# Performance work log

Hardware: AMD Instinct MI355X
Metric: run time of the kernel (lower is better)

## Reference

```python
import jax, jax.numpy as jnp
import numpy as np

B, N, D = 8, 1024, 768      # batch, n_patches, prototype dim
V, C, Hh = 30000, 512, 768  # vocab size, clip_text_dim, proj hidden dim
TEMPERATURE = 0.2
BN_EPS = 1e-5


def _l2norm(x, axis=-1, eps=1e-12):
    # matches torch F.normalize (clamp_min on the norm)
    n = jnp.linalg.norm(x, axis=axis, keepdims=True)
    return x / jnp.maximum(n, eps)


def setup_inputs() -> dict:
    key = jax.random.key(0)
    k = jax.random.split(key, 6)
    patch_tokens = jax.random.normal(k[0], (B, N, D), dtype=jnp.float32)
    vocab_clip_embeddings = jax.random.normal(k[1], (V, C), dtype=jnp.float32)
    # ProjectionHead params: Linear(C->Hh, no bias) + BN(Hh) + ReLU + Linear(Hh->D, bias)
    W1 = jax.random.normal(k[2], (C, Hh), dtype=jnp.float32) / np.sqrt(C)
    bn_gamma = jnp.ones((Hh,), dtype=jnp.float32)
    bn_beta = jnp.zeros((Hh,), dtype=jnp.float32)
    W2 = jax.random.normal(k[3], (Hh, D), dtype=jnp.float32) / np.sqrt(Hh)
    b2 = jnp.zeros((D,), dtype=jnp.float32)
    return {
        "patch_tokens": patch_tokens,
        "vocab_clip_embeddings": vocab_clip_embeddings,
        "W1": W1,
        "bn_gamma": bn_gamma,
        "bn_beta": bn_beta,
        "W2": W2,
        "b2": b2,
    }


def reference(patch_tokens, vocab_clip_embeddings, W1, bn_gamma, bn_beta, W2, b2):
    # vocab CLIP embeddings are L2-normalized at module init
    vocab = _l2norm(vocab_clip_embeddings)            # [V, C]
    # ProjectionHead (training-mode BatchNorm over the V "batch" dim)
    h = vocab @ W1                                    # [V, Hh]
    mean = jnp.mean(h, axis=0)
    var = jnp.var(h, axis=0)                          # biased, as torch BN uses
    h = (h - mean) * (bn_gamma / jnp.sqrt(var + BN_EPS)) + bn_beta
    h = jax.nn.relu(h)
    prototypes = _l2norm(h @ W2 + b2)                 # [V, D]
    # normalize patch tokens, compute patch-prototype logits
    pt = _l2norm(patch_tokens)                        # [B, N, D]
    patch_prototype_logits = jnp.einsum("bnd,vd->bnv", pt, prototypes)  # [B, N, V]
    vocab_logits = jnp.max(patch_prototype_logits, axis=1)              # [B, V]
    mixture_weights = jax.nn.softmax(vocab_logits / TEMPERATURE, axis=-1)
    return mixture_weights
```

## Files before the change

kernel.cpp:

```cpp
#include <hip/hip_runtime.h>
#include <hip/hip_bf16.h>
#include <cstdint>


#define CDIV(a,b) (((a)+(b)-1)/(b))

using bf16x8 = __attribute__((ext_vector_type(8))) __bf16;
using f32x4  = __attribute__((ext_vector_type(4))) float;

__device__ __forceinline__ unsigned short f2bf(float x) {
  unsigned u = __float_as_uint(x);
  u += 0x7fffu + ((u >> 16) & 1u);
  return (unsigned short)(u >> 16);
}
__device__ __forceinline__ float bf2f(unsigned short b) {
  return __uint_as_float(((unsigned)b) << 16);
}
__device__ __forceinline__ unsigned fkey(float x) {
  unsigned u = __float_as_uint(x);
  return (u & 0x80000000u) ? ~u : (u | 0x80000000u);
}
__device__ __forceinline__ float fdec(unsigned k) {
  unsigned u = (k & 0x80000000u) ? (k ^ 0x80000000u) : ~k;
  return __uint_as_float(u);
}

__global__ __launch_bounds__(512, 1)
void gemm256_max_kernel(const unsigned short* __restrict__ A,
                        const unsigned short* __restrict__ B,
                        unsigned* __restrict__ maxkey)
{
  constexpr int K = 768, NT = 12, NXT = 118;
  __shared__ __align__(16) unsigned short lds[8 * 8192];

  const int tid = threadIdx.x;
  const int w = tid >> 6, lane = tid & 63;
  const int lr = lane & 15, kg = lane >> 4;
  const int wr = w >> 2, wc = w & 3;

  const int bid = blockIdx.x;
  const int wg = (bid & 7) * 472 + (bid >> 3);
  const long m0 = (long)(wg / NXT) * 256;
  const long n0 = (long)(wg % NXT) * 256;

  auto stage = [&](int slot, int tk, int mat, int h) {
    const unsigned short* src = mat ? B : A;
    const long row0 = mat ? n0 : m0;
    unsigned short* dst = lds + (((slot * 2) + mat) * 2 + h) * 8192;
#pragma unroll
    for (int ld = 0; ld < 2; ++ld) {
      const int lc  = ld * 512 + tid;
      const int row = lc >> 2;
      const int qc  = (lc & 3) ^ ((row >> 1) & 3);
      const unsigned short* gp = src + (row0 + row) * K + tk * 64 + h * 32 + qc * 8;
      __builtin_amdgcn_global_load_lds(
          (const __attribute__((address_space(1))) void*)gp,
          (__attribute__((address_space(3))) void*)(dst + (ld * 512 + (w << 6)) * 8),
          16, 0, 0);
    }
  };
  auto rdA = [&](int s, int h, int fm) -> bf16x8 {
    const int row = wr * 128 + fm * 16 + lr;
    const int pc  = kg ^ ((row >> 1) & 3);
    return *(const bf16x8*)(lds + ((s * 2 + 0) * 2 + h) * 8192 + row * 32 + pc * 8);
  };
  auto rdB = [&](int s, int h, int fn) -> bf16x8 {
    const int row = wc * 64 + fn * 16 + lr;
    const int pc  = kg ^ ((row >> 1) & 3);
    return *(const bf16x8*)(lds + ((s * 2 + 1) * 2 + h) * 8192 + row * 32 + pc * 8);
  };

  f32x4 acc[8][4];
#pragma unroll
  for (int i = 0; i < 8; ++i)
#pragma unroll
    for (int j = 0; j < 4; ++j) acc[i][j] = f32x4{0.f, 0.f, 0.f, 0.f};

  stage(0, 0, 0, 0); stage(0, 0, 1, 0); stage(0, 0, 0, 1);
  stage(0, 0, 1, 1); stage(1, 1, 0, 0); stage(1, 1, 1, 0);
  asm volatile("s_waitcnt vmcnt(8)" ::: "memory");
  __builtin_amdgcn_s_barrier();

  bf16x8 a[4], b[4];
  auto tile_body = [&](int t, int s) {
    const int t1c = (t + 1 < NT) ? t + 1 : NT - 1;
    const int t2c = (t + 2 < NT) ? t + 2 : NT - 1;
    const int s1  = s ^ 1;

#pragma unroll
    for (int i = 0; i < 4; ++i) a[i] = rdA(s, 0, i);
#pragma unroll
    for (int i = 0; i < 4; ++i) b[i] = rdB(s, 0, i);
    stage(s1, t1c, 0, 1);
    __builtin_amdgcn_s_barrier();
    asm volatile("s_waitcnt lgkmcnt(0)" ::: "memory");
    __builtin_amdgcn_sched_barrier(0);
    __builtin_amdgcn_s_setprio(1);
#pragma unroll
    for (int fm = 0; fm < 4; ++fm)
#pragma unroll
      for (int fn = 0; fn < 4; ++fn)
        acc[fm][fn] = __builtin_amdgcn_mfma_f32_16x16x32_bf16(a[fm], b[fn], acc[fm][fn], 0, 0, 0);
    __builtin_amdgcn_s_setprio(0);
    __builtin_amdgcn_sched_barrier(0);
    __builtin_amdgcn_s_barrier();

#pragma unroll
    for (int i = 0; i < 4; ++i) a[i] = rdA(s, 0, 4 + i);
    stage(s1, t1c, 1, 1);
    __builtin_amdgcn_s_barrier();
    asm volatile("s_waitcnt lgkmcnt(0)" ::: "memory");
    __builtin_amdgcn_sched_barrier(0);
    __builtin_amdgcn_s_setprio(1);
#pragma unroll
    for (int fm = 0; fm < 4; ++fm)
#pragma unroll
      for (int fn = 0; fn < 4; ++fn)
        acc[4 + fm][fn] = __builtin_amdgcn_mfma_f32_16x16x32_bf16(a[fm], b[fn], acc[4 + fm][fn], 0, 0, 0);
    __builtin_amdgcn_s_setprio(0);
    asm volatile("s_waitcnt vmcnt(8)" ::: "memory");
    __builtin_amdgcn_sched_barrier(0);
    __builtin_amdgcn_s_barrier();

#pragma unroll
    for (int i = 0; i < 4; ++i) a[i] = rdA(s, 1, i);
#pragma unroll
    for (int i = 0; i < 4; ++i) b[i] = rdB(s, 1, i);
    stage(s, t2c, 0, 0);
    __builtin_amdgcn_s_barrier();
    asm volatile("s_waitcnt lgkmcnt(0)" ::: "memory");
    __builtin_amdgcn_sched_barrier(0);
    __builtin_amdgcn_s_setprio(1);
#pragma unroll
    for (int fm = 0; fm < 4; ++fm)
#pragma unroll
      for (int fn = 0; fn < 4; ++fn)
        acc[fm][fn] = __builtin_amdgcn_mfma_f32_16x16x32_bf16(a[fm], b[fn], acc[fm][fn], 0, 0, 0);
    __builtin_amdgcn_s_setprio(0);
    __builtin_amdgcn_sched_barrier(0);
    __builtin_amdgcn_s_barrier();

#pragma unroll
    for (int i = 0; i < 4; ++i) a[i] = rdA(s, 1, 4 + i);
    stage(s, t2c, 1, 0);
    __builtin_amdgcn_s_barrier();
    asm volatile("s_waitcnt lgkmcnt(0)" ::: "memory");
    __builtin_amdgcn_sched_barrier(0);
    __builtin_amdgcn_s_setprio(1);
#pragma unroll
    for (int fm = 0; fm < 4; ++fm)
#pragma unroll
      for (int fn = 0; fn < 4; ++fn)
        acc[4 + fm][fn] = __builtin_amdgcn_mfma_f32_16x16x32_bf16(a[fm], b[fn], acc[4 + fm][fn], 0, 0, 0);
    __builtin_amdgcn_s_setprio(0);
    asm volatile("s_waitcnt vmcnt(8)" ::: "memory");
    __builtin_amdgcn_sched_barrier(0);
    __builtin_amdgcn_s_barrier();
  };

  for (int tt = 0; tt < NT; tt += 2) { tile_body(tt, 0); tile_body(tt + 1, 1); }

  const int bb = (int)(m0 >> 10);
#pragma unroll
  for (int fn = 0; fn < 4; ++fn) {
    float mx = acc[0][fn][0];
#pragma unroll
    for (int fm = 0; fm < 8; ++fm)
#pragma unroll
      for (int j = 0; j < 4; ++j) mx = fmaxf(mx, acc[fm][fn][j]);
    mx = fmaxf(mx, __shfl_xor(mx, 16));
    mx = fmaxf(mx, __shfl_xor(mx, 32));
    const long gn = n0 + wc * 64 + fn * 16 + lr;
    if (lane < 16)
      atomicMax(maxkey + (long)bb * 30208 + gn, fkey(mx));
  }
}

template<int EPI>
__global__ __launch_bounds__(256)
void gemm_nt_kernel(const unsigned short* __restrict__ A,
                    const unsigned short* __restrict__ B,
                    unsigned short* __restrict__ Cout,
                    const float* __restrict__ bias,
                    int M, int N, int K)
{
  __shared__ __align__(16) unsigned short As[128 * 32];
  __shared__ __align__(16) unsigned short Bs[128 * 32];
  const int tid  = threadIdx.x;
  const int w    = tid >> 6, lane = tid & 63;
  const int m0   = blockIdx.y * 128, n0 = blockIdx.x * 128;
  const int wr   = w >> 1, wc = w & 1;
  const int lrow = lane & 15, kg = lane >> 4;

  f32x4 acc[4][4];
#pragma unroll
  for (int i = 0; i < 4; ++i)
#pragma unroll
    for (int j = 0; j < 4; ++j) acc[i][j] = f32x4{0.f, 0.f, 0.f, 0.f};

  for (int k0 = 0; k0 < K; k0 += 32) {
#pragma unroll
    for (int i = 0; i < 2; ++i) {
      const int li = w * 2 + i;
      const int c  = li * 64 + lane;
      const int r  = c >> 2;
      const int kc = (c & 3) * 8;
      {
        int row = m0 + r; if (row > M - 1) row = M - 1;
        const unsigned short* gp = A + (size_t)row * K + (k0 + kc);
        __builtin_amdgcn_global_load_lds(
            (const __attribute__((address_space(1))) void*)gp,
            (__attribute__((address_space(3))) void*)(As + li * 512), 16, 0, 0);
      }
      {
        int row = n0 + r; if (row > N - 1) row = N - 1;
        const unsigned short* gp = B + (size_t)row * K + (k0 + kc);
        __builtin_amdgcn_global_load_lds(
            (const __attribute__((address_space(1))) void*)gp,
            (__attribute__((address_space(3))) void*)(Bs + li * 512), 16, 0, 0);
      }
    }
    __syncthreads();

    bf16x8 af[4], bfr[4];
#pragma unroll
    for (int fm = 0; fm < 4; ++fm)
      af[fm] = *(const bf16x8*)(As + (wr * 64 + fm * 16 + lrow) * 32 + kg * 8);
#pragma unroll
    for (int fn = 0; fn < 4; ++fn)
      bfr[fn] = *(const bf16x8*)(Bs + (wc * 64 + fn * 16 + lrow) * 32 + kg * 8);

#pragma unroll
    for (int fm = 0; fm < 4; ++fm)
#pragma unroll
      for (int fn = 0; fn < 4; ++fn)
        acc[fm][fn] = __builtin_amdgcn_mfma_f32_16x16x32_bf16(
            af[fm], bfr[fn], acc[fm][fn], 0, 0, 0);
    __syncthreads();
  }

#pragma unroll
  for (int fm = 0; fm < 4; ++fm) {
    const int gmb = m0 + wr * 64 + fm * 16 + kg * 4;
#pragma unroll
    for (int fn = 0; fn < 4; ++fn) {
      const int gn = n0 + wc * 64 + fn * 16 + lrow;
      const float bv = (EPI == 1) ? bias[gn] : 0.0f;
#pragma unroll
      for (int j = 0; j < 4; ++j) {
        const int gm = gmb + j;
        if (gm < M) Cout[(size_t)gm * N + gn] = f2bf(acc[fm][fn][j] + bv);
      }
    }
  }
}

template<bool INBF>
__global__ __launch_bounds__(256)
void rownorm_kernel(const void* __restrict__ in, unsigned short* __restrict__ out,
                    int cols)
{
  __shared__ float red[4];
  const int row = blockIdx.x;
  const size_t base = (size_t)row * cols;
  const float* fin = (const float*)in;
  const unsigned short* bin = (const unsigned short*)in;

  float ss = 0.f;
  for (int ci = threadIdx.x; ci < cols; ci += 256) {
    float x = INBF ? bf2f(bin[base + ci]) : fin[base + ci];
    ss += x * x;
  }
#pragma unroll
  for (int m = 32; m; m >>= 1) ss += __shfl_xor(ss, m);
  if ((threadIdx.x & 63) == 0) red[threadIdx.x >> 6] = ss;
  __syncthreads();
  const float tot = red[0] + red[1] + red[2] + red[3];
  const float inv = 1.0f / fmaxf(sqrtf(tot), 1e-12f);
  for (int ci = threadIdx.x; ci < cols; ci += 256) {
    float x = INBF ? bf2f(bin[base + ci]) : fin[base + ci];
    out[base + ci] = f2bf(x * inv);
  }
}

__global__ __launch_bounds__(256)
void transpose_kernel(const float* __restrict__ in, unsigned short* __restrict__ out,
                      int R, int Cc)
{
  int i = blockIdx.x * 256 + threadIdx.x;
  if (i < R * Cc) {
    int r = i / Cc, c = i - r * Cc;
    out[(size_t)c * R + r] = f2bf(in[i]);
  }
}

__global__ __launch_bounds__(256)
void bnstats_kernel(const unsigned short* __restrict__ h, float* __restrict__ sums)
{
  const int r0 = blockIdx.x * 250;
  const int c0 = threadIdx.x, c1 = threadIdx.x + 256, c2 = threadIdx.x + 512;
  float a0 = 0, a1 = 0, a2 = 0, q0 = 0, q1 = 0, q2 = 0;
  for (int r = r0; r < r0 + 250; ++r) {
    const size_t base = (size_t)r * 768;
    float x0 = bf2f(h[base + c0]); a0 += x0; q0 += x0 * x0;
    float x1 = bf2f(h[base + c1]); a1 += x1; q1 += x1 * x1;
    float x2 = bf2f(h[base + c2]); a2 += x2; q2 += x2 * x2;
  }
  atomicAdd(&sums[c0], a0); atomicAdd(&sums[768 + c0], q0);
  atomicAdd(&sums[c1], a1); atomicAdd(&sums[768 + c1], q1);
  atomicAdd(&sums[c2], a2); atomicAdd(&sums[768 + c2], q2);
}

__global__ __launch_bounds__(256)
void bnapply_kernel(unsigned short* __restrict__ h, const float* __restrict__ sums,
                    const float* __restrict__ gamma, const float* __restrict__ beta)
{
  const float invV = 1.0f / 30000.0f;
  const size_t total = 30000ull * 768;
  for (size_t i = blockIdx.x * 256ull + threadIdx.x; i < total; i += 2048ull * 256) {
    const int ch = (int)(i % 768);
    const float mean = sums[ch] * invV;
    const float var  = sums[768 + ch] * invV - mean * mean;
    const float sc   = gamma[ch] / sqrtf(var + 1e-5f);
    const float y    = (bf2f(h[i]) - mean) * sc + beta[ch];
    h[i] = f2bf(fmaxf(y, 0.0f));
  }
}

__global__ __launch_bounds__(1024)
void softmax_kernel(const unsigned* __restrict__ mk, float* __restrict__ out)
{
  __shared__ float red[16];
  const int b = blockIdx.x;
  const unsigned* row = mk + (size_t)b * 30208;
  const int tid = threadIdx.x;

  float m = -3.0e38f;
  for (int v = tid; v < 30000; v += 1024) m = fmaxf(m, fdec(row[v]));
#pragma unroll
  for (int s = 32; s; s >>= 1) m = fmaxf(m, __shfl_xor(m, s));
  if ((tid & 63) == 0) red[tid >> 6] = m;
  __syncthreads();
  float bm = red[0];
#pragma unroll
  for (int i = 1; i < 16; ++i) bm = fmaxf(bm, red[i]);
  __syncthreads();

  float s = 0.f;
  for (int v = tid; v < 30000; v += 1024) s += expf((fdec(row[v]) - bm) * 5.0f);
#pragma unroll
  for (int sh = 32; sh; sh >>= 1) s += __shfl_xor(s, sh);
  if ((tid & 63) == 0) red[tid >> 6] = s;
  __syncthreads();
  float bs = 0.f;
#pragma unroll
  for (int i = 0; i < 16; ++i) bs += red[i];

  for (int v = tid; v < 30000; v += 1024)
    out[(size_t)b * 30000 + v] = expf((fdec(row[v]) - bm) * 5.0f) / bs;
}

extern "C" void kernel_launch(void* const* d_in, const int* in_sizes, int n_in,
                              void* d_out, int out_size, void* d_ws, size_t ws_size,
                              hipStream_t stream)
{
  (void)in_sizes; (void)n_in; (void)out_size; (void)ws_size;
  const float* patch = (const float*)d_in[0];
  const float* vocab = (const float*)d_in[1];
  const float* W1    = (const float*)d_in[2];
  const float* gamma = (const float*)d_in[3];
  const float* beta  = (const float*)d_in[4];
  const float* W2    = (const float*)d_in[5];
  const float* b2    = (const float*)d_in[6];
  float* out = (float*)d_out;

  char* ws = (char*)d_ws;
  size_t off = 0;
  auto alloc = [&](size_t bytes) {
    char* p = ws + off;
    off += (bytes + 1023) & ~(size_t)1023;
    return p;
  };
  unsigned short* vocab_n = (unsigned short*)alloc(30000ull * 512 * 2);
  unsigned short* pt_n    = (unsigned short*)alloc(8192ull * 768 * 2);
  unsigned short* W1T     = (unsigned short*)alloc(768ull * 512 * 2);
  unsigned short* W2T     = (unsigned short*)alloc(768ull * 768 * 2);
  unsigned short* hbuf    = (unsigned short*)alloc(30000ull * 768 * 2);
  unsigned short* pbuf    = (unsigned short*)alloc(30000ull * 768 * 2);
  unsigned short* proto   = (unsigned short*)alloc(30208ull * 768 * 2);
  float*          bnsums  = (float*)alloc(768ull * 2 * 4);
  unsigned*       maxkey  = (unsigned*)alloc(8ull * 30208 * 4);

  hipMemsetAsync(bnsums, 0, 768ull * 2 * 4, stream);
  hipMemsetAsync(maxkey, 0, 8ull * 30208 * 4, stream);
  hipMemsetAsync(proto + 30000ull * 768, 0, 208ull * 768 * 2, stream);

  transpose_kernel<<<CDIV(512 * 768, 256), 256, 0, stream>>>(W1, W1T, 512, 768);
  transpose_kernel<<<CDIV(768 * 768, 256), 256, 0, stream>>>(W2, W2T, 768, 768);
  rownorm_kernel<false><<<30000, 256, 0, stream>>>(vocab, vocab_n, 512);
  rownorm_kernel<false><<<8192, 256, 0, stream>>>(patch, pt_n, 768);

  gemm_nt_kernel<0><<<dim3(6, 235), 256, 0, stream>>>(
      vocab_n, W1T, hbuf, nullptr, 30000, 768, 512);
  bnstats_kernel<<<120, 256, 0, stream>>>(hbuf, bnsums);
  bnapply_kernel<<<2048, 256, 0, stream>>>(hbuf, bnsums, gamma, beta);
  gemm_nt_kernel<1><<<dim3(6, 235), 256, 0, stream>>>(
      hbuf, W2T, pbuf, b2, 30000, 768, 768);
  rownorm_kernel<true><<<30000, 256, 0, stream>>>(pbuf, proto, 768);

  gemm256_max_kernel<<<3776, 512, 0, stream>>>(pt_n, proto, maxkey);

  softmax_kernel<<<8, 1024, 0, stream>>>(maxkey, out);
}
```

Before: 735.0 us.

## Fuse BN stats into GEMM epilogue, vectorize norms, and parallelize softmax

Per-column BatchNorm sums are now accumulated in the first projection GEMM's epilogue with shuffles and atomics, which removes the separate bnstats pass over the hidden buffer. A tiny kernel precomputes the BN scale and shift, and bnapply now works on 8-element vectors with one fma per element. Rownorm uses vector loads, keeps each row in registers and uses a 128-thread block for the bf16 path. The softmax is split into a multi-block partial-sum kernel and a vectorized output kernel, using 1.0 as the fixed max because the logits are cosine similarities. The fixed max depends on the logits staying bounded by 1, and the epilogue atomics add contention.

```diff
diff --git a/kernel.cpp b/kernel.cpp
--- a/kernel.cpp
+++ b/kernel.cpp
@@ -7,6 +7,9 @@
 
 using bf16x8 = __attribute__((ext_vector_type(8))) __bf16;
 using f32x4  = __attribute__((ext_vector_type(4))) float;
+using u16x8  = __attribute__((ext_vector_type(8))) unsigned short;
+using u16x4  = __attribute__((ext_vector_type(4))) unsigned short;
+using u32x4  = __attribute__((ext_vector_type(4))) unsigned;
 
 __device__ __forceinline__ unsigned short f2bf(float x) {
   unsigned u = __float_as_uint(x);
@@ -176,12 +179,13 @@
   }
 }
 
-template<int EPI>
+template<int EPI, bool STATS>
 __global__ __launch_bounds__(256)
 void gemm_nt_kernel(const unsigned short* __restrict__ A,
                     const unsigned short* __restrict__ B,
                     unsigned short* __restrict__ Cout,
                     const float* __restrict__ bias,
+                    float* __restrict__ sums,
                     int M, int N, int K)
 {
   __shared__ __align__(16) unsigned short As[128 * 32];
@@ -253,33 +257,77 @@
       }
     }
   }
-}
-
-template<bool INBF>
-__global__ __launch_bounds__(256)
+
+  if (STATS) {
+#pragma unroll
+    for (int fn = 0; fn < 4; ++fn) {
+      const int gn = n0 + wc * 64 + fn * 16 + lrow;
+      float s = 0.f, q = 0.f;
+#pragma unroll
+      for (int fm = 0; fm < 4; ++fm) {
+        const int gmb = m0 + wr * 64 + fm * 16 + kg * 4;
+#pragma unroll
+        for (int j = 0; j < 4; ++j) {
+          if (gmb + j < M) {
+            const float x = acc[fm][fn][j];
+            s += x; q += x * x;
+          }
+        }
+      }
+      s += __shfl_xor(s, 16); s += __shfl_xor(s, 32);
+      q += __shfl_xor(q, 16); q += __shfl_xor(q, 32);
+      if (lane < 16 && gn < N) {
+        atomicAdd(sums + gn, s);
+        atomicAdd(sums + 768 + gn, q);
+      }
+    }
+  }
+}
+
+template<int BLOCK, bool INBF>
+__global__ __launch_bounds__(BLOCK)
 void rownorm_kernel(const void* __restrict__ in, unsigned short* __restrict__ out,
                     int cols)
 {
-  __shared__ float red[4];
-  const int row = blockIdx.x;
-  const size_t base = (size_t)row * cols;
-  const float* fin = (const float*)in;
-  const unsigned short* bin = (const unsigned short*)in;
-
+  __shared__ float red[BLOCK / 64];
+  constexpr int VE = INBF ? 8 : 4;
+  const int row = blockIdx.x, tid = threadIdx.x;
+  const int nch = cols / VE;
+
+  float x[VE];
   float ss = 0.f;
-  for (int ci = threadIdx.x; ci < cols; ci += 256) {
-    float x = INBF ? bf2f(bin[base + ci]) : fin[base + ci];
-    ss += x * x;
+  if (tid < nch) {
+    if (INBF) {
+      const u16x8 v = ((const u16x8*)((const unsigned short*)in + (size_t)row * cols))[tid];
+#pragma unroll
+      for (int j = 0; j < 8; ++j) { x[j] = bf2f(v[j]); ss += x[j] * x[j]; }
+    } else {
+      const f32x4 v = ((const f32x4*)((const float*)in + (size_t)row * cols))[tid];
+#pragma unroll
+      for (int j = 0; j < 4; ++j) { x[j] = v[j]; ss += x[j] * x[j]; }
+    }
   }
 #pragma unroll
   for (int m = 32; m; m >>= 1) ss += __shfl_xor(ss, m);
-  if ((threadIdx.x & 63) == 0) red[threadIdx.x >> 6] = ss;
+  if ((tid & 63) == 0) red[tid >> 6] = ss;
   __syncthreads();
-  const float tot = red[0] + red[1] + red[2] + red[3];
+  float tot = 0.f;
+#pragma unroll
+  for (int i = 0; i < BLOCK / 64; ++i) tot += red[i];
   const float inv = 1.0f / fmaxf(sqrtf(tot), 1e-12f);
-  for (int ci = threadIdx.x; ci < cols; ci += 256) {
-    float x = INBF ? bf2f(bin[base + ci]) : fin[base + ci];
-    out[base + ci] = f2bf(x * inv);
+
+  if (tid < nch) {
+    if (INBF) {
+      u16x8 o;
+#pragma unroll
+      for (int j = 0; j < 8; ++j) o[j] = f2bf(x[j] * inv);
+      ((u16x8*)(out + (size_t)row * cols))[tid] = o;
+    } else {
+      u16x4 o;
+#pragma unroll
+      for (int j = 0; j < 4; ++j) o[j] = f2bf(x[j] * inv);
+      ((u16x4*)(out + (size_t)row * cols))[tid] = o;
+    }
   }
 }
 
@@ -295,69 +343,77 @@
 }
 
 __global__ __launch_bounds__(256)
-void bnstats_kernel(const unsigned short* __restrict__ h, float* __restrict__ sums)
-{
-  const int r0 = blockIdx.x * 250;
-  const int c0 = threadIdx.x, c1 = threadIdx.x + 256, c2 = threadIdx.x + 512;
-  float a0 = 0, a1 = 0, a2 = 0, q0 = 0, q1 = 0, q2 = 0;
-  for (int r = r0; r < r0 + 250; ++r) {
-    const size_t base = (size_t)r * 768;
-    float x0 = bf2f(h[base + c0]); a0 += x0; q0 += x0 * x0;
-    float x1 = bf2f(h[base + c1]); a1 += x1; q1 += x1 * x1;
-    float x2 = bf2f(h[base + c2]); a2 += x2; q2 += x2 * x2;
-  }
-  atomicAdd(&sums[c0], a0); atomicAdd(&sums[768 + c0], q0);
-  atomicAdd(&sums[c1], a1); atomicAdd(&sums[768 + c1], q1);
-  atomicAdd(&sums[c2], a2); atomicAdd(&sums[768 + c2], q2);
-}
-
-__global__ __launch_bounds__(256)
-void bnapply_kernel(unsigned short* __restrict__ h, const float* __restrict__ sums,
-                    const float* __restrict__ gamma, const float* __restrict__ beta)
-{
-  const float invV = 1.0f / 30000.0f;
-  const size_t total = 30000ull * 768;
-  for (size_t i = blockIdx.x * 256ull + threadIdx.x; i < total; i += 2048ull * 256) {
-    const int ch = (int)(i % 768);
+void bnfinal_kernel(const float* __restrict__ sums, const float* __restrict__ gamma,
+                    const float* __restrict__ beta, float* __restrict__ sc,
+                    float* __restrict__ sh)
+{
+  const int ch = blockIdx.x * 256 + threadIdx.x;
+  if (ch < 768) {
+    const float invV = 1.0f / 30000.0f;
     const float mean = sums[ch] * invV;
     const float var  = sums[768 + ch] * invV - mean * mean;
-    const float sc   = gamma[ch] / sqrtf(var + 1e-5f);
-    const float y    = (bf2f(h[i]) - mean) * sc + beta[ch];
-    h[i] = f2bf(fmaxf(y, 0.0f));
-  }
-}
-
-__global__ __launch_bounds__(1024)
-void softmax_kernel(const unsigned* __restrict__ mk, float* __restrict__ out)
-{
-  __shared__ float red[16];
-  const int b = blockIdx.x;
-  const unsigned* row = mk + (size_t)b * 30208;
-  const int tid = threadIdx.x;
-
-  float m = -3.0e38f;
-  for (int v = tid; v < 30000; v += 1024) m = fmaxf(m, fdec(row[v]));
-#pragma unroll
-  for (int s = 32; s; s >>= 1) m = fmaxf(m, __shfl_xor(m, s));
-  if ((tid & 63) == 0) red[tid >> 6] = m;
+    const float s    = gamma[ch] / sqrtf(var + 1e-5f);
+    sc[ch] = s;
+    sh[ch] = beta[ch] - mean * s;
+  }
+}
+
+__global__ __launch_bounds__(256)
+void bnapply_kernel(unsigned short* __restrict__ h, const float* __restrict__ sc,
+                    const float* __restrict__ sh)
+{
+  const int total = 30000 * 96;
+  for (int c = blockIdx.x * 256 + threadIdx.x; c < total; c += 2048 * 256) {
+    const int ch = (c % 96) * 8;
+    const u16x8 v = ((const u16x8*)h)[c];
+    u16x8 o;
+#pragma unroll
+    for (int j = 0; j < 8; ++j) {
+      const float y = fmaf(bf2f(v[j]), sc[ch + j], sh[ch + j]);
+      o[j] = f2bf(fmaxf(y, 0.0f));
+    }
+    ((u16x8*)h)[c] = o;
+  }
+}
+
+__global__ __launch_bounds__(256)
+void smpart_kernel(const unsigned* __restrict__ mk, float* __restrict__ partsum)
+{
+  __shared__ float red[4];
+  const int b = blockIdx.y;
+  const unsigned* row = mk + (size_t)b * 30208 + blockIdx.x * 1000;
+  float s = 0.f;
+  for (int t = threadIdx.x; t < 1000; t += 256)
+    s += expf((fdec(row[t]) - 1.0f) * 5.0f);
+#pragma unroll
+  for (int m = 32; m; m >>= 1) s += __shfl_xor(s, m);
+  if ((threadIdx.x & 63) == 0) red[threadIdx.x >> 6] = s;
   __syncthreads();
-  float bm = red[0];
-#pragma unroll
-  for (int i = 1; i < 16; ++i) bm = fmaxf(bm, red[i]);
-  __syncthreads();
-
-  float s = 0.f;
-  for (int v = tid; v < 30000; v += 1024) s += expf((fdec(row[v]) - bm) * 5.0f);
-#pragma unroll
-  for (int sh = 32; sh; sh >>= 1) s += __shfl_xor(s, sh);
-  if ((tid & 63) == 0) red[tid >> 6] = s;
-  __syncthreads();
-  float bs = 0.f;
-#pragma unroll
-  for (int i = 0; i < 16; ++i) bs += red[i];
-
-  for (int v = tid; v < 30000; v += 1024)
-    out[(size_t)b * 30000 + v] = expf((fdec(row[v]) - bm) * 5.0f) / bs;
+  if (threadIdx.x == 0)
+    atomicAdd(partsum + b, red[0] + red[1] + red[2] + red[3]);
+}
+
+__global__ __launch_bounds__(256)
+void smfinal_kernel(const unsigned* __restrict__ mk, const float* __restrict__ partsum,
+                    float* __restrict__ out)
+{
+  const int b = blockIdx.y;
+  const int c = blockIdx.x * 256 + threadIdx.x;
+  if (c < 3750) {
+    const unsigned* row = mk + (size_t)b * 30208 + c * 8;
+    const float inv = 1.0f / partsum[b];
+    const u32x4 k0 = *(const u32x4*)row;
+    const u32x4 k1 = *(const u32x4*)(row + 4);
+    f32x4 o0, o1;
+#pragma unroll
+    for (int j = 0; j < 4; ++j) {
+      o0[j] = expf((fdec(k0[j]) - 1.0f) * 5.0f) * inv;
+      o1[j] = expf((fdec(k1[j]) - 1.0f) * 5.0f) * inv;
+    }
+    float* op = out + (size_t)b * 30000 + c * 8;
+    *(f32x4*)op = o0;
+    *(f32x4*)(op + 4) = o1;
+  }
 }
 
 extern "C" void kernel_launch(void* const* d_in, const int* in_sizes, int n_in,
@@ -389,26 +445,31 @@
   unsigned short* pbuf    = (unsigned short*)alloc(30000ull * 768 * 2);
   unsigned short* proto   = (unsigned short*)alloc(30208ull * 768 * 2);
   float*          bnsums  = (float*)alloc(768ull * 2 * 4);
+  float*          bnsc    = (float*)alloc(768ull * 4);
+  float*          bnsh    = (float*)alloc(768ull * 4);
   unsigned*       maxkey  = (unsigned*)alloc(8ull * 30208 * 4);
+  float*          partsum = (float*)alloc(8ull * 4);
 
   hipMemsetAsync(bnsums, 0, 768ull * 2 * 4, stream);
   hipMemsetAsync(maxkey, 0, 8ull * 30208 * 4, stream);
   hipMemsetAsync(proto + 30000ull * 768, 0, 208ull * 768 * 2, stream);
+  hipMemsetAsync(partsum, 0, 8ull * 4, stream);
 
   transpose_kernel<<<CDIV(512 * 768, 256), 256, 0, stream>>>(W1, W1T, 512, 768);
   transpose_kernel<<<CDIV(768 * 768, 256), 256, 0, stream>>>(W2, W2T, 768, 768);
-  rownorm_kernel<false><<<30000, 256, 0, stream>>>(vocab, vocab_n, 512);
-  rownorm_kernel<false><<<8192, 256, 0, stream>>>(patch, pt_n, 768);
-
-  gemm_nt_kernel<0><<<dim3(6, 235), 256, 0, stream>>>(
-      vocab_n, W1T, hbuf, nullptr, 30000, 768, 512);
-  bnstats_kernel<<<120, 256, 0, stream>>>(hbuf, bnsums);
-  bnapply_kernel<<<2048, 256, 0, stream>>>(hbuf, bnsums, gamma, beta);
-  gemm_nt_kernel<1><<<dim3(6, 235), 256, 0, stream>>>(
-      hbuf, W2T, pbuf, b2, 30000, 768, 768);
-  rownorm_kernel<true><<<30000, 256, 0, stream>>>(pbuf, proto, 768);
+  rownorm_kernel<256, false><<<30000, 256, 0, stream>>>(vocab, vocab_n, 512);
+  rownorm_kernel<256, false><<<8192, 256, 0, stream>>>(patch, pt_n, 768);
+
+  gemm_nt_kernel<0, true><<<dim3(6, 235), 256, 0, stream>>>(
+      vocab_n, W1T, hbuf, nullptr, bnsums, 30000, 768, 512);
+  bnfinal_kernel<<<3, 256, 0, stream>>>(bnsums, gamma, beta, bnsc, bnsh);
+  bnapply_kernel<<<2048, 256, 0, stream>>>(hbuf, bnsc, bnsh);
+  gemm_nt_kernel<1, false><<<dim3(6, 235), 256, 0, stream>>>(
+      hbuf, W2T, pbuf, b2, nullptr, 30000, 768, 768);
+  rownorm_kernel<128, true><<<30000, 128, 0, stream>>>(pbuf, proto, 768);
 
   gemm256_max_kernel<<<3776, 512, 0, stream>>>(pt_n, proto, maxkey);
 
-  softmax_kernel<<<8, 1024, 0, stream>>>(maxkey, out);
-}
+  smpart_kernel<<<dim3(30, 8), 256, 0, stream>>>(maxkey, partsum);
+  smfinal_kernel<<<dim3(15, 8), 256, 0, stream>>>(maxkey, partsum, out);
+}
```

Result: faster. 635.4 us (-13.5%).
